# Performance work log

Hardware: AMD Instinct MI355X
Metric: run time of the kernel (lower is better)

## Reference

```python
import jax, jax.numpy as jnp
import numpy as np

D_MODEL = 768
NUM_HEADS = 12
D_K = D_MODEL // NUM_HEADS


def setup_inputs() -> dict:
    key = jax.random.key(0)
    ks = jax.random.split(key, 7)
    B, S = 4, 2048
    query = jax.random.normal(ks[0], (B, S, D_MODEL), dtype=jnp.float32)
    key_t = jax.random.normal(ks[1], (B, S, D_MODEL), dtype=jnp.float32)
    value = jax.random.normal(ks[2], (B, S, D_MODEL), dtype=jnp.float32)
    lim = 1.0 / np.sqrt(D_MODEL)
    Wq = jax.random.uniform(ks[3], (D_MODEL, D_MODEL), jnp.float32, -lim, lim)  # torch Linear weight [out,in]
    bq = jax.random.uniform(ks[4], (D_MODEL,), jnp.float32, -lim, lim)
    Wo = jax.random.uniform(ks[5], (D_MODEL, D_MODEL), jnp.float32, -lim, lim)
    bo = jax.random.uniform(ks[6], (D_MODEL,), jnp.float32, -lim, lim)
    return {"query": query, "key": key_t, "value": value,
            "Wq": Wq, "bq": bq, "Wo": Wo, "bo": bo}


def _proj_heads(x, W, b):
    # x: [B,S,D] -> [B,H,S,d_k]; torch Linear: x @ W.T + b
    B, S, _ = x.shape
    y = x @ W.T + b
    return y.reshape(B, S, NUM_HEADS, D_K).transpose(0, 2, 1, 3)


def reference(query, key, value, Wq, bq, Wo, bo):
    # Faithful to source: linear_q is used for q, k AND v (source bug).
    q = _proj_heads(query, Wq, bq)
    k = _proj_heads(key, Wq, bq)
    v = _proj_heads(value, Wq, bq)
    scale = 1.0 / jnp.sqrt(jnp.asarray(D_K, q.dtype))
    scores = jnp.einsum('bhqd,bhkd->bhqk', q, k) * scale  # [B,H,S,S]
    attn = jax.nn.softmax(scores, axis=-1)
    out = jnp.einsum('bhqk,bhkd->bhqd', attn, v)  # [B,H,S,d_k]
    B, H, S, dk = out.shape
    out = out.transpose(0, 2, 1, 3).reshape(B, S, H * dk)
    return out @ Wo.T + bo
```

## Files before the change

kernel.cpp:

```cpp
#include <hip/hip_runtime.h>
#include <math.h>

typedef _Float16 f16x8 __attribute__((ext_vector_type(8)));
typedef _Float16 f16x4 __attribute__((ext_vector_type(4)));
typedef float    f32x4 __attribute__((ext_vector_type(4)));
typedef unsigned short us4 __attribute__((ext_vector_type(4)));
typedef unsigned int u32;
typedef unsigned int u32x4 __attribute__((ext_vector_type(4)));

constexpr int DM = 768, NH = 12, DK = 64, SEQ = 2048, BB = 4;
constexpr int MROWS = BB * SEQ;
constexpr size_t XELE = (size_t)MROWS * DM;
constexpr size_t WELE = (size_t)DM * DM;

constexpr size_t OFF_X16  = 0;
constexpr size_t OFF_W16  = 3 * XELE;
constexpr size_t OFF_WO16 = OFF_W16 + WELE;
constexpr size_t OFF_QKV  = OFF_WO16 + WELE;
constexpr size_t OFF_ATT  = OFF_QKV + 3 * XELE;
constexpr size_t TOT_CVT  = OFF_QKV;


constexpr float QSCALE = 0.125f * 1.44269504f;
constexpr float MSEED = -8.0f;

__device__ __forceinline__ void gload16(const _Float16* g, _Float16* l) {
    __builtin_amdgcn_global_load_lds(
        (const __attribute__((address_space(1))) unsigned int*)g,
        (__attribute__((address_space(3))) unsigned int*)l, 16, 0, 0);
}

__device__ __forceinline__ uint2 pack4(float a, float b, float c, float d) {
    uint2 r;
    r.x = __builtin_bit_cast(u32, __builtin_amdgcn_cvt_pkrtz(a, b));
    r.y = __builtin_bit_cast(u32, __builtin_amdgcn_cvt_pkrtz(c, d));
    return r;
}

__global__ __launch_bounds__(256) void cvt_kernel(
    const float* __restrict__ q, const float* __restrict__ k,
    const float* __restrict__ v, const float* __restrict__ wq,
    const float* __restrict__ wo, _Float16* __restrict__ dst)
{
    const size_t i = ((size_t)blockIdx.x * 256 + threadIdx.x) * 4;
    if (i >= TOT_CVT) return;
    const float* src; size_t base;
    if      (i < XELE)            { src = q;  base = 0; }
    else if (i < 2 * XELE)        { src = k;  base = XELE; }
    else if (i < 3 * XELE)        { src = v;  base = 2 * XELE; }
    else if (i < OFF_WO16)        { src = wq; base = OFF_W16; }
    else                          { src = wo; base = OFF_WO16; }
    const float4 f = *(const float4*)(src + (i - base));
    _Float16 h4[4] = {(_Float16)f.x, (_Float16)f.y, (_Float16)f.z, (_Float16)f.w};
    *(us4*)(dst + i) = *(us4*)h4;
}

template <int MODE>
__global__ __launch_bounds__(256) void mfma_gemm(
    const _Float16* __restrict__ Xbase, const _Float16* __restrict__ Wmat,
    const float* __restrict__ bias, void* __restrict__ Yout)
{
    __shared__ _Float16 smem[128 * 136];

    const int bid = blockIdx.x;
    const int xs  = bid & 7;
    const int rr  = bid >> 3;
    const int m_blk = ((rr & 7) << 3) | xs;
    const int tt  = rr >> 3;
    const int n_blk = tt % 6;
    const int z     = tt / 6;

    const int tid  = threadIdx.x;
    const int w    = tid >> 6, lane = tid & 63;
    const int cl   = lane & 15;
    const int g    = lane >> 4;
    const int m0   = m_blk * 128, n0 = n_blk * 128;
    const _Float16* X = Xbase + (size_t)z * XELE;

    const int wr = w >> 1, wc = w & 1;
    const int lrow = lane >> 2;
    const int lcol = (lane & 3) * 8;

    f32x4 acc[4][4] = {};

    constexpr int NK = DM / 32;
#pragma unroll
    for (int t = 0; t < 2; ++t) {
        const int c = w + t * 4;
        gload16(X    + (size_t)(m0 + c * 16 + lrow) * DM + lcol, &smem[c * 512]);
        gload16(Wmat + (size_t)(n0 + c * 16 + lrow) * DM + lcol, &smem[4096 + c * 512]);
    }

    int cur = 0;
    for (int ki = 0; ki < NK; ++ki) {
        __syncthreads();
        if (ki + 1 < NK) {
            const int kn = (ki + 1) * 32;
            _Float16* dst = &smem[(cur ^ 1) * 8192];
#pragma unroll
            for (int t = 0; t < 2; ++t) {
                const int c = w + t * 4;
                gload16(X    + (size_t)(m0 + c * 16 + lrow) * DM + kn + lcol, &dst[c * 512]);
                gload16(Wmat + (size_t)(n0 + c * 16 + lrow) * DM + kn + lcol, &dst[4096 + c * 512]);
            }
        }
        const _Float16* As = &smem[cur * 8192];
        const _Float16* Bs = As + 4096;

        f16x8 a[4], bfr[4];
#pragma unroll
        for (int mt = 0; mt < 4; ++mt)
            a[mt] = *(const f16x8*)&As[(wr * 64 + mt * 16 + cl) * 32 + g * 8];
#pragma unroll
        for (int nt = 0; nt < 4; ++nt)
            bfr[nt] = *(const f16x8*)&Bs[(wc * 64 + nt * 16 + cl) * 32 + g * 8];
#pragma unroll
        for (int mt = 0; mt < 4; ++mt)
#pragma unroll
            for (int nt = 0; nt < 4; ++nt)
                acc[mt][nt] = __builtin_amdgcn_mfma_f32_16x16x32_f16(
                    a[mt], bfr[nt], acc[mt][nt], 0, 0, 0);
        cur ^= 1;
    }

    __syncthreads();
    const float sc = (z == 0) ? QSCALE : 1.0f;
#pragma unroll
    for (int nt = 0; nt < 4; ++nt) {
        const int col = wc * 64 + nt * 16 + cl;
        const float bv = bias[n0 + col];
#pragma unroll
        for (int mt = 0; mt < 4; ++mt)
#pragma unroll
            for (int r = 0; r < 4; ++r) {
                const int row = wr * 64 + mt * 16 + g * 4 + r;
                const _Float16 hv = (_Float16)((acc[mt][nt][r] + bv) * sc);
                if (z == 2) smem[col * 136 + row] = hv;
                else        smem[row * 136 + col] = hv;
            }
    }
    __syncthreads();

    _Float16* Yz = (_Float16*)Yout + (size_t)z * XELE;
#pragma unroll
    for (int it = 0; it < 8; ++it) {
        const int idx = tid + it * 256;
        const int row = idx >> 4;
        const int grp = idx & 15;
        const f16x8 vv = *(const f16x8*)&smem[row * 136 + grp * 8];
        if (z == 2) {
            const int f  = n0 + row, hh = f >> 6, d = f & 63;
            const int gm = m0 + grp * 8;
            const int bb = gm >> 11, s = gm & (SEQ - 1);
            const int ssw = (s & ~63) | ((((s >> 3) & 7) ^ (d & 7)) << 3);
            *(f16x8*)&Yz[(((size_t)bb * NH + hh) * DK + d) * SEQ + ssw] = vv;
        } else {
            const int gm = m0 + row;
            const int bb = gm >> 11, s = gm & (SEQ - 1);
            const int n  = n0 + grp * 8, hh = n >> 6, d0 = n & 63;
            const int dsw = ((((d0 >> 3) ^ (s & 7)) & 7) << 3);
            *(f16x8*)&Yz[(((size_t)bb * NH + hh) * SEQ + s) * DK + dsw] = vv;
        }
    }
}

__global__ __launch_bounds__(256) void gemm_out(
    const _Float16* __restrict__ X,
    const _Float16* __restrict__ Wmat,
    const float* __restrict__ bias, float* __restrict__ Y)
{
    __shared__ _Float16 smem[2 * 6144];

    const int bid = blockIdx.x;
    const int xs  = bid & 7;
    const int rr  = bid >> 3;
    const int m_blk = ((rr & 15) << 3) | xs;
    const int n_blk = rr >> 4;

    const int tid = threadIdx.x;
    const int w = tid >> 6, lane = tid & 63;
    const int cl = lane & 15, g = lane >> 4;
    const int m0 = m_blk * 64, n0 = n_blk * 128;

    const int lrow = lane >> 2;
    const int lcol = (lane & 3) * 8;

    f32x4 acc[4][2] = {};

    constexpr int NK = DM / 32;
    gload16(X    + (size_t)(m0 + w * 16 + lrow) * DM + lcol, &smem[w * 512]);
    gload16(Wmat + (size_t)(n0 + w * 16 + lrow) * DM + lcol, &smem[2048 + w * 512]);
    gload16(Wmat + (size_t)(n0 + (w + 4) * 16 + lrow) * DM + lcol, &smem[2048 + (w + 4) * 512]);

    int cur = 0;
    for (int ki = 0; ki < NK; ++ki) {
        __syncthreads();
        if (ki + 1 < NK) {
            const int kn = (ki + 1) * 32;
            _Float16* dst = &smem[(cur ^ 1) * 6144];
            gload16(X    + (size_t)(m0 + w * 16 + lrow) * DM + kn + lcol, &dst[w * 512]);
            gload16(Wmat + (size_t)(n0 + w * 16 + lrow) * DM + kn + lcol, &dst[2048 + w * 512]);
            gload16(Wmat + (size_t)(n0 + (w + 4) * 16 + lrow) * DM + kn + lcol, &dst[2048 + (w + 4) * 512]);
        }
        const _Float16* As = &smem[cur * 6144];
        const _Float16* Bs = As + 2048;

        f16x8 a[4], bfr[2];
#pragma unroll
        for (int mt = 0; mt < 4; ++mt)
            a[mt] = *(const f16x8*)&As[(mt * 16 + cl) * 32 + g * 8];
#pragma unroll
        for (int nt = 0; nt < 2; ++nt)
            bfr[nt] = *(const f16x8*)&Bs[(w * 32 + nt * 16 + cl) * 32 + g * 8];
#pragma unroll
        for (int mt = 0; mt < 4; ++mt)
#pragma unroll
            for (int nt = 0; nt < 2; ++nt)
                acc[mt][nt] = __builtin_amdgcn_mfma_f32_16x16x32_f16(
                    a[mt], bfr[nt], acc[mt][nt], 0, 0, 0);
        cur ^= 1;
    }

#pragma unroll
    for (int nt = 0; nt < 2; ++nt) {
        const int col = n0 + w * 32 + nt * 16 + cl;
        const float bv = bias[col];
#pragma unroll
        for (int mt = 0; mt < 4; ++mt)
#pragma unroll
            for (int r = 0; r < 4; ++r) {
                const int row = m0 + mt * 16 + g * 4 + r;
                Y[(size_t)row * DM + col] = acc[mt][nt][r] + bv;
            }
    }
}

__global__ __launch_bounds__(256) void flash4(
    const _Float16* __restrict__ qkv, _Float16* __restrict__ attno)
{
    __shared__ _Float16 KsB[2 * 64 * 64];
    __shared__ _Float16 VtB[2 * 64 * 64];

    const int bid = blockIdx.x;
    const int xs  = bid & 7;
    const int rr  = bid >> 3;
    const int p   = (rr % 6) * 8 + xs;
    const int qtb = rr / 6;
    const int h   = p % NH, b = p / NH;
    const int q0  = qtb * 128;

    const int tid = threadIdx.x;
    const int w = tid >> 6, lane = tid & 63;
    const int cl = lane & 15, g = lane >> 4;
    const int swz = cl & 7;

    const size_t headoff = ((size_t)b * NH + h) * SEQ * DK;
    const _Float16* Qg = qkv + headoff;
    const _Float16* Kg = qkv + XELE + headoff;
    const _Float16* Vg = qkv + 2 * XELE + headoff;

    const int ldr = lane >> 3, ldc = (lane & 7) * 8;

#pragma unroll
    for (int t = 0; t < 2; ++t) {
        const int c = w * 2 + t;
        gload16(Kg + (size_t)(c * 8 + ldr) * DK + ldc, &KsB[c * 512]);
        gload16(Vg + (size_t)(c * 8 + ldr) * SEQ + ldc, &VtB[c * 512]);
    }

    f16x8 qf[2][2];
#pragma unroll
    for (int qt = 0; qt < 2; ++qt)
#pragma unroll
        for (int ks = 0; ks < 2; ++ks)
            qf[qt][ks] = *(const f16x8*)(
                Qg + (size_t)(q0 + w * 32 + qt * 16 + cl) * DK
                   + (((ks * 4 + g) ^ swz) << 3));

    float l_run[2] = {0.f, 0.f};
    f32x4 acc[2][4] = {};

    int cur = 0;
    for (int j0 = 0; j0 < SEQ; j0 += 64) {
        __syncthreads();
        if (j0 + 64 < SEQ) {
            const int jn = j0 + 64;
            _Float16* Kd = &KsB[(cur ^ 1) * 4096];
            _Float16* Vd = &VtB[(cur ^ 1) * 4096];
#pragma unroll
            for (int t = 0; t < 2; ++t) {
                const int c = w * 2 + t;
                gload16(Kg + (size_t)(jn + c * 8 + ldr) * DK + ldc, &Kd[c * 512]);
                gload16(Vg + (size_t)(c * 8 + ldr) * SEQ + jn + ldc, &Vd[c * 512]);
            }
        }
        const _Float16* Ks = &KsB[cur * 4096];
        const _Float16* Vt = &VtB[cur * 4096];

        f16x8 kf[4][2];
#pragma unroll
        for (int kt = 0; kt < 4; ++kt)
#pragma unroll
            for (int ks = 0; ks < 2; ++ks)
                kf[kt][ks] = *(const f16x8*)&Ks[(kt * 16 + cl) * 64
                                                + (((ks * 4 + g) ^ swz) << 3)];

        uint2 pk[2][4];
#pragma unroll
        for (int qt = 0; qt < 2; ++qt) {
            float ps = 0.f;
#pragma unroll
            for (int kt = 0; kt < 4; ++kt) {
                f32x4 s = {MSEED, MSEED, MSEED, MSEED};
#pragma unroll
                for (int ks = 0; ks < 2; ++ks)
                    s = __builtin_amdgcn_mfma_f32_16x16x32_f16(
                        kf[kt][ks], qf[qt][ks], s, 0, 0, 0);
                const float p0 = __builtin_amdgcn_exp2f(s[0]);
                const float p1 = __builtin_amdgcn_exp2f(s[1]);
                const float p2 = __builtin_amdgcn_exp2f(s[2]);
                const float p3 = __builtin_amdgcn_exp2f(s[3]);
                ps += (p0 + p1) + (p2 + p3);
                pk[qt][kt] = pack4(p0, p1, p2, p3);
            }
            l_run[qt] += ps;
        }

        f16x8 pf[2][2];
#pragma unroll
        for (int qt = 0; qt < 2; ++qt)
#pragma unroll
            for (int ks = 0; ks < 2; ++ks) {
                u32 a0 = pk[qt][2 * ks].x, b0 = pk[qt][2 * ks + 1].x;
                u32 a1 = pk[qt][2 * ks].y, b1 = pk[qt][2 * ks + 1].y;
                {
                    auto r = __builtin_amdgcn_permlane32_swap(a0, b0, false, false);
                    a0 = r[0]; b0 = r[1];
                }
                {
                    auto r = __builtin_amdgcn_permlane16_swap(a0, b0, false, false);
                    a0 = r[0]; b0 = r[1];
                }
                {
                    auto r = __builtin_amdgcn_permlane32_swap(a1, b1, false, false);
                    a1 = r[0]; b1 = r[1];
                }
                {
                    auto r = __builtin_amdgcn_permlane16_swap(a1, b1, false, false);
                    a1 = r[0]; b1 = r[1];
                }
                u32x4 wds = {a0, a1, b0, b1};
                pf[qt][ks] = __builtin_bit_cast(f16x8, wds);
            }

        f16x8 vf[4][2];
#pragma unroll
        for (int dt = 0; dt < 4; ++dt)
#pragma unroll
            for (int ks = 0; ks < 2; ++ks)
                vf[dt][ks] = *(const f16x8*)&Vt[(dt * 16 + cl) * 64
                                                + (((ks * 4 + g) ^ swz) << 3)];
#pragma unroll
        for (int qt = 0; qt < 2; ++qt)
#pragma unroll
            for (int ks = 0; ks < 2; ++ks)
#pragma unroll
                for (int dt = 0; dt < 4; ++dt)
                    acc[qt][dt] = __builtin_amdgcn_mfma_f32_16x16x32_f16(
                        vf[dt][ks], pf[qt][ks], acc[qt][dt], 0, 0, 0);
        cur ^= 1;
    }

#pragma unroll
    for (int qt = 0; qt < 2; ++qt) {
        float l = l_run[qt];
        l += __shfl_xor(l, 16);
        l += __shfl_xor(l, 32);
        const float inv = 1.0f / l;
        const int q = q0 + w * 32 + qt * 16 + cl;
#pragma unroll
        for (int dt = 0; dt < 4; ++dt) {
            uint2 pk2 = pack4(acc[qt][dt][0] * inv, acc[qt][dt][1] * inv,
                              acc[qt][dt][2] * inv, acc[qt][dt][3] * inv);
            *(uint2*)&attno[((size_t)b * SEQ + q) * DM + h * DK + dt * 16 + g * 4] = pk2;
        }
    }
}

extern "C" void kernel_launch(void* const* d_in, const int* in_sizes, int n_in,
                              void* d_out, int out_size, void* d_ws, size_t ws_size,
                              hipStream_t stream) {
    const float* q  = (const float*)d_in[0];
    const float* k  = (const float*)d_in[1];
    const float* v  = (const float*)d_in[2];
    const float* Wq = (const float*)d_in[3];
    const float* bq = (const float*)d_in[4];
    const float* Wo = (const float*)d_in[5];
    const float* bo = (const float*)d_in[6];

    _Float16* ws16  = (_Float16*)d_ws;
    _Float16* x16   = ws16 + OFF_X16;
    _Float16* w16   = ws16 + OFF_W16;
    _Float16* wo16  = ws16 + OFF_WO16;
    _Float16* qkv16 = ws16 + OFF_QKV;
    _Float16* att16 = ws16 + OFF_ATT;

    cvt_kernel<<<(int)(TOT_CVT / 1024), 256, 0, stream>>>(q, k, v, Wq, Wo, ws16);

    mfma_gemm<0><<<1152, 256, 0, stream>>>(x16, w16, bq, qkv16);

    flash4<<<768, 256, 0, stream>>>(qkv16, att16);

    gemm_out<<<768, 256, 0, stream>>>(att16, wo16, bo, (float*)d_out);
}
```

Baseline: 257.5 us.

## Fuse fp32-to-fp16 activation conversion into QKV projection GEMM loads

The separate conversion pass over the q/k/v activations is removed. The QKV GEMM now reads fp32 activations directly into registers, converts them to fp16 and writes them into shared memory after the MFMA work for the current tile. Only the weights still go through a small conversion kernel. This saves one full read and write of the three activation tensors plus a launch. In exchange the A-tile prefetch moves from async global-to-LDS loads to register-staged loads, which raises register pressure and doubles the bytes the GEMM reads for A.

```diff
diff --git a/kernel.cpp b/kernel.cpp
--- a/kernel.cpp
+++ b/kernel.cpp
@@ -18,7 +18,7 @@
 constexpr size_t OFF_WO16 = OFF_W16 + WELE;
 constexpr size_t OFF_QKV  = OFF_WO16 + WELE;
 constexpr size_t OFF_ATT  = OFF_QKV + 3 * XELE;
-constexpr size_t TOT_CVT  = OFF_QKV;
+constexpr size_t TOT_CVTW = 2 * WELE;
 
 
 constexpr float QSCALE = 0.125f * 1.44269504f;
@@ -37,28 +37,23 @@
     return r;
 }
 
-__global__ __launch_bounds__(256) void cvt_kernel(
-    const float* __restrict__ q, const float* __restrict__ k,
-    const float* __restrict__ v, const float* __restrict__ wq,
-    const float* __restrict__ wo, _Float16* __restrict__ dst)
+__global__ __launch_bounds__(256) void cvt_w(
+    const float* __restrict__ wq, const float* __restrict__ wo,
+    _Float16* __restrict__ dst)
 {
     const size_t i = ((size_t)blockIdx.x * 256 + threadIdx.x) * 4;
-    if (i >= TOT_CVT) return;
-    const float* src; size_t base;
-    if      (i < XELE)            { src = q;  base = 0; }
-    else if (i < 2 * XELE)        { src = k;  base = XELE; }
-    else if (i < 3 * XELE)        { src = v;  base = 2 * XELE; }
-    else if (i < OFF_WO16)        { src = wq; base = OFF_W16; }
-    else                          { src = wo; base = OFF_WO16; }
+    if (i >= TOT_CVTW) return;
+    const float* src = (i < WELE) ? wq : wo;
+    const size_t base = (i < WELE) ? 0 : WELE;
     const float4 f = *(const float4*)(src + (i - base));
     _Float16 h4[4] = {(_Float16)f.x, (_Float16)f.y, (_Float16)f.z, (_Float16)f.w};
     *(us4*)(dst + i) = *(us4*)h4;
 }
 
-template <int MODE>
-__global__ __launch_bounds__(256) void mfma_gemm(
-    const _Float16* __restrict__ Xbase, const _Float16* __restrict__ Wmat,
-    const float* __restrict__ bias, void* __restrict__ Yout)
+__global__ __launch_bounds__(256) void gemm_qkv(
+    const float* __restrict__ q32, const float* __restrict__ k32,
+    const float* __restrict__ v32, const _Float16* __restrict__ Wmat,
+    const float* __restrict__ bias, _Float16* __restrict__ Yout)
 {
     __shared__ _Float16 smem[128 * 136];
 
@@ -75,7 +70,7 @@
     const int cl   = lane & 15;
     const int g    = lane >> 4;
     const int m0   = m_blk * 128, n0 = n_blk * 128;
-    const _Float16* X = Xbase + (size_t)z * XELE;
+    const float* Xf = (z == 0) ? q32 : (z == 1) ? k32 : v32;
 
     const int wr = w >> 1, wc = w & 1;
     const int lrow = lane >> 2;
@@ -84,26 +79,47 @@
     f32x4 acc[4][4] = {};
 
     constexpr int NK = DM / 32;
-#pragma unroll
-    for (int t = 0; t < 2; ++t) {
-        const int c = w + t * 4;
-        gload16(X    + (size_t)(m0 + c * 16 + lrow) * DM + lcol, &smem[c * 512]);
-        gload16(Wmat + (size_t)(n0 + c * 16 + lrow) * DM + lcol, &smem[4096 + c * 512]);
+
+    {
+        float4 av[2][2];
+#pragma unroll
+        for (int t = 0; t < 2; ++t) {
+            const int c = w + t * 4;
+            const float* srcA = Xf + (size_t)(m0 + c * 16 + lrow) * DM + lcol;
+            av[t][0] = *(const float4*)srcA;
+            av[t][1] = *(const float4*)(srcA + 4);
+            gload16(Wmat + (size_t)(n0 + c * 16 + lrow) * DM + lcol, &smem[4096 + c * 512]);
+        }
+#pragma unroll
+        for (int t = 0; t < 2; ++t) {
+            const int c = w + t * 4;
+            _Float16 h8[8] = {
+                (_Float16)av[t][0].x, (_Float16)av[t][0].y,
+                (_Float16)av[t][0].z, (_Float16)av[t][0].w,
+                (_Float16)av[t][1].x, (_Float16)av[t][1].y,
+                (_Float16)av[t][1].z, (_Float16)av[t][1].w};
+            *(f16x8*)&smem[c * 512 + lane * 8] = *(f16x8*)h8;
+        }
     }
 
     int cur = 0;
     for (int ki = 0; ki < NK; ++ki) {
         __syncthreads();
-        if (ki + 1 < NK) {
+        const bool pre = (ki + 1 < NK);
+        float4 av[2][2];
+        if (pre) {
             const int kn = (ki + 1) * 32;
             _Float16* dst = &smem[(cur ^ 1) * 8192];
 #pragma unroll
             for (int t = 0; t < 2; ++t) {
                 const int c = w + t * 4;
-                gload16(X    + (size_t)(m0 + c * 16 + lrow) * DM + kn + lcol, &dst[c * 512]);
+                const float* srcA = Xf + (size_t)(m0 + c * 16 + lrow) * DM + kn + lcol;
+                av[t][0] = *(const float4*)srcA;
+                av[t][1] = *(const float4*)(srcA + 4);
                 gload16(Wmat + (size_t)(n0 + c * 16 + lrow) * DM + kn + lcol, &dst[4096 + c * 512]);
             }
         }
+
         const _Float16* As = &smem[cur * 8192];
         const _Float16* Bs = As + 4096;
 
@@ -120,6 +136,20 @@
             for (int nt = 0; nt < 4; ++nt)
                 acc[mt][nt] = __builtin_amdgcn_mfma_f32_16x16x32_f16(
                     a[mt], bfr[nt], acc[mt][nt], 0, 0, 0);
+
+        if (pre) {
+            _Float16* dst = &smem[(cur ^ 1) * 8192];
+#pragma unroll
+            for (int t = 0; t < 2; ++t) {
+                const int c = w + t * 4;
+                _Float16 h8[8] = {
+                    (_Float16)av[t][0].x, (_Float16)av[t][0].y,
+                    (_Float16)av[t][0].z, (_Float16)av[t][0].w,
+                    (_Float16)av[t][1].x, (_Float16)av[t][1].y,
+                    (_Float16)av[t][1].z, (_Float16)av[t][1].w};
+                *(f16x8*)&dst[c * 512 + lane * 8] = *(f16x8*)h8;
+            }
+        }
         cur ^= 1;
     }
 
@@ -141,7 +171,7 @@
     }
     __syncthreads();
 
-    _Float16* Yz = (_Float16*)Yout + (size_t)z * XELE;
+    _Float16* Yz = Yout + (size_t)z * XELE;
 #pragma unroll
     for (int it = 0; it < 8; ++it) {
         const int idx = tid + it * 256;
@@ -399,15 +429,14 @@
     const float* bo = (const float*)d_in[6];
 
     _Float16* ws16  = (_Float16*)d_ws;
-    _Float16* x16   = ws16 + OFF_X16;
     _Float16* w16   = ws16 + OFF_W16;
     _Float16* wo16  = ws16 + OFF_WO16;
     _Float16* qkv16 = ws16 + OFF_QKV;
     _Float16* att16 = ws16 + OFF_ATT;
 
-    cvt_kernel<<<(int)(TOT_CVT / 1024), 256, 0, stream>>>(q, k, v, Wq, Wo, ws16);
-
-    mfma_gemm<0><<<1152, 256, 0, stream>>>(x16, w16, bq, qkv16);
+    cvt_w<<<(int)(TOT_CVTW / 1024), 256, 0, stream>>>(Wq, Wo, w16);
+
+    gemm_qkv<<<1152, 256, 0, stream>>>(q, k, v, w16, bq, qkv16);
 
     flash4<<<768, 256, 0, stream>>>(qkv16, att16);
 
```

Result: slower. 275.6 us (+7.0%).
